# Kernel optimization log

Measured on AMD Instinct MI355X. Metric: run time of the kernel, lower is better.

Reference implementation:

```python
import jax, jax.numpy as jnp
import numpy as np

B, S, D = 2, 2048, 1024
H = 16
HD = D // H  # 64


def setup_inputs() -> dict:
    key = jax.random.key(0)
    k1, k2, k3, k4, k5, k6 = jax.random.split(key, 6)
    hidden_states = jax.random.normal(k1, (B, S, D), dtype=jnp.float32)
    attention_mask = jax.random.randint(k2, (B, S), 0, 2, dtype=jnp.int32)
    scale = 1.0 / np.sqrt(D)
    Wq = jax.random.normal(k3, (D, D), dtype=jnp.float32) * scale
    bq = jax.random.normal(k4, (D,), dtype=jnp.float32) * 0.02
    Wk = jax.random.normal(k5, (D, D), dtype=jnp.float32) * scale
    bk = jax.random.normal(k6, (D,), dtype=jnp.float32) * 0.02
    return {"hidden_states": hidden_states, "attention_mask": attention_mask,
            "Wq": Wq, "bq": bq, "Wk": Wk, "bk": bk}


def _split_heads(x):
    # [B, S, D] -> [B, H, S, HD]
    b, s, _ = x.shape
    return x.reshape(b, s, H, HD).transpose(0, 2, 1, 3)


def reference(hidden_states, attention_mask, Wq, bq, Wk, bk):
    dh = jnp.sqrt(jnp.float32(HD))
    q = _split_heads(hidden_states @ Wq + bq)            # [B,H,S,HD]
    k = _split_heads(hidden_states @ Wk + bk)            # [B,H,S,HD]
    v = q + k                                            # value = Q + K
    k_t = -jax.nn.log_sigmoid(-k)                        # negate the logsigmoid(-K) transform
    scores = jnp.einsum('bhqd,bhkd->bhqk', q, k_t) / dh  # [B,H,S,S]
    # mask applied on the QUERY axis (dim 2), broadcast over key axis (faithful to source)
    mask = (attention_mask[:, None, :, None] == 0)       # [B,1,S,1]
    scores = jnp.where(mask, jnp.float32(-10000.0), scores)
    probs = jax.nn.softmax(scores, axis=-1)              # dropout: eval mode (identity)
    ctx = jnp.einsum('bhqk,bhkd->bhqd', probs, v)        # [B,H,S,HD]
    ctx = ctx.transpose(0, 2, 1, 3).reshape(B, S, D)
    return ctx
```

## Files before the change

kernel.cpp:

```cpp
#include <hip/hip_runtime.h>
#include <hip/hip_bf16.h>

#define B_ 2
#define S_ 2048
#define D_ 1024
#define H_ 16
#define HD_ 64

typedef __attribute__((ext_vector_type(8))) short short8;
typedef __attribute__((ext_vector_type(4))) short short4v;
typedef __attribute__((ext_vector_type(4))) float float4v;

typedef const __attribute__((address_space(1))) void* gas_ptr;
typedef __attribute__((address_space(3))) void* las_ptr;

static __device__ inline void gl_lds16(const void* g, void* l) {
  __builtin_amdgcn_global_load_lds((gas_ptr)g, (las_ptr)l, 16, 0, 0);
}

static __device__ inline short f2bs(float x) {
  __hip_bfloat16 h = __float2bfloat16(x);
  union { __hip_bfloat16 h; short s; } u; u.h = h; return u.s;
}
static __device__ inline float bs2f(short s) {
  union { short s; __hip_bfloat16 h; } u; u.s = s; return __bfloat162float(u.h);
}
static __device__ inline short4v pk4(float a, float b, float c, float d) {
  union { __hip_bfloat162 h[2]; short4v s; } u;
  u.h[0] = __float22bfloat162_rn(float2{a, b});
  u.h[1] = __float22bfloat162_rn(float2{c, d});
  return u.s;
}

static __device__ inline float4v mfma32(short8 a, short8 b, float4v c) {
  return __builtin_amdgcn_mfma_f32_16x16x32_bf16(a, b, c, 0, 0, 0);
}
static __device__ inline float4v mfma16(short4v a, short4v b, float4v c) {
  return __builtin_amdgcn_mfma_f32_16x16x16bf16_1k(a, b, c, 0, 0, 0);
}

__global__ __launch_bounds__(256) void prep(
    const float* __restrict__ hs, __hip_bfloat16* __restrict__ hsb,
    const float* __restrict__ Wq, const float* __restrict__ Wk,
    __hip_bfloat16* __restrict__ Wqt, __hip_bfloat16* __restrict__ Wkt) {
  __shared__ float t[64][65];
  const int id = blockIdx.x;
  if (id < 2048) {
    const size_t i = ((size_t)id * 256 + threadIdx.x) * 8;
    const float4v a0 = ((const float4v*)(hs + i))[0];
    const float4v a1 = ((const float4v*)(hs + i))[1];
    short8 s;
#pragma unroll
    for (int j = 0; j < 4; ++j) { s[j] = f2bs(a0[j]); s[4 + j] = f2bs(a1[j]); }
    *(short8*)(hsb + i) = s;
    return;
  }
  const int bid = id - 2048;
  const float* W = (bid >> 8) ? Wk : Wq;
  __hip_bfloat16* Wt = (bid >> 8) ? Wkt : Wqt;
  const int n0 = (bid & 15) * 64, k0 = ((bid >> 4) & 15) * 64;
  const int c = threadIdx.x & 63, r0 = threadIdx.x >> 6;
  for (int i = 0; i < 16; ++i) {
    const int r = i * 4 + r0;
    t[c][r] = W[(size_t)(k0 + r) * D_ + n0 + c];
  }
  __syncthreads();
  for (int i = 0; i < 16; ++i) {
    const int rr = i * 4 + r0;
    Wt[(size_t)(n0 + rr) * D_ + k0 + c] = __float2bfloat16(t[rr][c]);
  }
}

__global__ __launch_bounds__(256, 2) void gemm_fused(
    const __hip_bfloat16* __restrict__ hsb,
    const __hip_bfloat16* __restrict__ Wqt, const __hip_bfloat16* __restrict__ Wkt,
    const float* __restrict__ bq, const float* __restrict__ bk,
    __hip_bfloat16* __restrict__ q_out, __hip_bfloat16* __restrict__ kt_out,
    __hip_bfloat16* __restrict__ vT) {
  const int id = blockIdx.x;
  const int mt = (id & 7) * 8 + ((id >> 3) & 7);
  const int nt = id >> 6;
  const int n0 = nt * 128, m0 = mt * 64;
  __shared__ __hip_bfloat16 As[2][64 * 32];
  __shared__ __hip_bfloat16 Bq[2][128 * 32];
  __shared__ __hip_bfloat16 Bk[2][128 * 32];
  const int tid = threadIdx.x, wid = tid >> 6, lane = tid & 63;
  const int wm = (wid >> 1) * 32, wn = (wid & 1) * 64;
  const int l15 = lane & 15, l4 = lane >> 4;
  const float4v zz = {0.f, 0.f, 0.f, 0.f};
  float4v accq[2][4], acck[2][4];
  for (int i = 0; i < 2; ++i)
    for (int j = 0; j < 4; ++j) { accq[i][j] = zz; acck[i][j] = zz; }
  const int lrow = wid * 16 + (lane >> 2);
  const int lk8 = (((lane & 3) ^ ((lane >> 3) & 3)) * 8);
  {
    gl_lds16(hsb + (size_t)(m0 + lrow) * D_ + lk8, As[0] + wid * 512);
    gl_lds16(Wqt + (size_t)(n0 + lrow) * D_ + lk8, Bq[0] + wid * 512);
    gl_lds16(Wqt + (size_t)(n0 + 64 + lrow) * D_ + lk8, Bq[0] + 2048 + wid * 512);
    gl_lds16(Wkt + (size_t)(n0 + lrow) * D_ + lk8, Bk[0] + wid * 512);
    gl_lds16(Wkt + (size_t)(n0 + 64 + lrow) * D_ + lk8, Bk[0] + 2048 + wid * 512);
  }
  int p = 0;
  for (int kb = 0; kb < 32; ++kb) {
    __syncthreads();
    if (kb < 31) {
      const int kc = (kb + 1) * 32 + lk8;
      gl_lds16(hsb + (size_t)(m0 + lrow) * D_ + kc, As[p ^ 1] + wid * 512);
      gl_lds16(Wqt + (size_t)(n0 + lrow) * D_ + kc, Bq[p ^ 1] + wid * 512);
      gl_lds16(Wqt + (size_t)(n0 + 64 + lrow) * D_ + kc, Bq[p ^ 1] + 2048 + wid * 512);
      gl_lds16(Wkt + (size_t)(n0 + lrow) * D_ + kc, Bk[p ^ 1] + wid * 512);
      gl_lds16(Wkt + (size_t)(n0 + 64 + lrow) * D_ + kc, Bk[p ^ 1] + 2048 + wid * 512);
    }
    short8 af[2], bfq[4], bfk[4];
    const int fo = ((l4 ^ ((l15 >> 1) & 3)) * 8);
    for (int rt = 0; rt < 2; ++rt)
      af[rt] = *(const short8*)(As[p] + (wm + rt * 16 + l15) * 32 + fo);
    for (int ct = 0; ct < 4; ++ct) {
      bfq[ct] = *(const short8*)(Bq[p] + (wn + ct * 16 + l15) * 32 + fo);
      bfk[ct] = *(const short8*)(Bk[p] + (wn + ct * 16 + l15) * 32 + fo);
    }
    for (int rt = 0; rt < 2; ++rt)
      for (int ct = 0; ct < 4; ++ct) {
        accq[rt][ct] = mfma32(af[rt], bfq[ct], accq[rt][ct]);
        acck[rt][ct] = mfma32(af[rt], bfk[ct], acck[rt][ct]);
      }
    p ^= 1;
  }
  float bvq[4], bvk[4];
  for (int ct = 0; ct < 4; ++ct) {
    bvq[ct] = bq[n0 + wn + ct * 16 + l15];
    bvk[ct] = bk[n0 + wn + ct * 16 + l15];
  }
  for (int rt = 0; rt < 2; ++rt)
    for (int ct = 0; ct < 4; ++ct) {
      const int col = n0 + wn + ct * 16 + l15;
      const int h = col >> 6, d = col & 63;
      const int rowb = m0 + wm + rt * 16 + l4 * 4;
      short4v vv;
      for (int r = 0; r < 4; ++r) {
        const int row = rowb + r;
        const float qv = accq[rt][ct][r] + bvq[ct];
        const float kv = acck[rt][ct][r] + bvk[ct];
        const float sp = fmaxf(kv, 0.f) + __logf(1.f + __expf(-fabsf(kv)));
        q_out[(size_t)row * D_ + col] = __float2bfloat16(qv);
        kt_out[(size_t)row * D_ + col] = __float2bfloat16(sp);
        vv[r] = f2bs(qv + kv);
      }
      const int b = rowb >> 11, s = rowb & 2047;
      const int sw = (s & ~63) | (((s >> 4) & 3) << 2) | (((s >> 2) & 3) << 4);
      *(short4v*)(vT + ((size_t)(b * H_ + h) * HD_ + d) * S_ + sw) = vv;
    }
}

__global__ __launch_bounds__(256, 2) void attn(
    const __hip_bfloat16* __restrict__ qb, const __hip_bfloat16* __restrict__ ktb,
    const __hip_bfloat16* __restrict__ vT, const int* __restrict__ mask,
    float* __restrict__ out) {
  __shared__ short smem[32768];
  const int id = blockIdx.x;
  const int xcd = id & 7;
  const int rest = id >> 3;
  const int q0 = (rest & 15) * 128;
  const int hb = (rest >> 4) * 8 + xcd;
  const int h = hb >> 1, b = hb & 1;
  const int tid = threadIdx.x, wid = tid >> 6, lane = tid & 63;
  const int l15 = lane & 15, l4 = lane >> 4;
  const int qs = (wid & 1) * 64;
  const int kh = wid >> 1;
  const __hip_bfloat16* qh = qb + (size_t)b * S_ * D_ + h * HD_;
  const __hip_bfloat16* kh_ = ktb + (size_t)b * S_ * D_ + h * HD_;
  const __hip_bfloat16* vh = vT + (size_t)(b * H_ + h) * HD_ * S_;
  const int srow = tid >> 2;
  const int b0 = tid & 3;
  const int ssw = ((srow & 1) << 2) | ((srow >> 1) & 3);
  const int w0 = srow * 64 + ((b0 ^ ssw) * 8);
  const int w1 = srow * 64 + (((b0 + 4) ^ ssw) * 8);

  const float SC = 0.125f * 1.44269504f;
  short8 bq0[4], bq1[4];
#pragma unroll
  for (int T = 0; T < 4; ++T) {
    const int qr = q0 + qs + T * 16 + l15;
    const float mq = (mask[b * S_ + qr] != 0) ? SC : 0.f;
    const short8 r0 = *(const short8*)(qh + (size_t)qr * D_ + l4 * 8);
    const short8 r1 = *(const short8*)(qh + (size_t)qr * D_ + 32 + l4 * 8);
#pragma unroll
    for (int j = 0; j < 8; ++j) {
      bq0[T][j] = f2bs(bs2f(r0[j]) * mq);
      bq1[T][j] = f2bs(bs2f(r1[j]) * mq);
    }
  }

  const int lsw = ((l15 & 1) << 2) | ((l15 >> 1) & 3);
  const int ak0off = l15 * 64 + ((l4 ^ lsw) * 8);
  const int ak1off = l15 * 64 + (((l4 + 4) ^ lsw) * 8);
  const int vb0off = ((2 * l4) ^ lsw) * 8;
  const int vb1off = ((2 * l4 + 1) ^ lsw) * 8;

  const float4v zz = {0.f, 0.f, 0.f, 0.f};
  float4v oacc[4][4];
#pragma unroll
  for (int T = 0; T < 4; ++T)
#pragma unroll
    for (int dt = 0; dt < 4; ++dt) oacc[T][dt] = zz;
  float4v ls[4] = {zz, zz, zz, zz};

  short8 gk0[2], gk1[2], gv0[2], gv1[2];
#pragma unroll
  for (int u = 0; u < 2; ++u) {
    gk0[u] = *(const short8*)(kh_ + (size_t)(u * 64 + srow) * D_ + b0 * 8);
    gk1[u] = *(const short8*)(kh_ + (size_t)(u * 64 + srow) * D_ + b0 * 8 + 32);
    gv0[u] = *(const short8*)(vh + (size_t)srow * S_ + u * 64 + b0 * 8);
    gv1[u] = *(const short8*)(vh + (size_t)srow * S_ + u * 64 + b0 * 8 + 32);
  }

  int pb = 0;
  for (int c = 0; c < 16; ++c) {
    short* bufp = smem + pb * 16384;
#pragma unroll
    for (int u = 0; u < 2; ++u) {
      *(short8*)(bufp + u * 4096 + w0) = gk0[u];
      *(short8*)(bufp + u * 4096 + w1) = gk1[u];
      *(short8*)(bufp + 8192 + u * 4096 + w0) = gv0[u];
      *(short8*)(bufp + 8192 + u * 4096 + w1) = gv1[u];
    }
    __syncthreads();
    if (c < 15) {
      const int kb = (c + 1) * 128;
#pragma unroll
      for (int u = 0; u < 2; ++u) {
        gk0[u] = *(const short8*)(kh_ + (size_t)(kb + u * 64 + srow) * D_ + b0 * 8);
        gk1[u] = *(const short8*)(kh_ + (size_t)(kb + u * 64 + srow) * D_ + b0 * 8 + 32);
        gv0[u] = *(const short8*)(vh + (size_t)srow * S_ + kb + u * 64 + b0 * 8);
        gv1[u] = *(const short8*)(vh + (size_t)srow * S_ + kb + u * 64 + b0 * 8 + 32);
      }
    }
    const short* kbase = bufp + kh * 4096;
    const short* vbase = bufp + 8192 + kh * 4096;
    short4v pf[4][4];
#pragma unroll
    for (int t = 0; t < 4; ++t) {
      const short8 ak0 = *(const short8*)(kbase + t * 1024 + ak0off);
      const short8 ak1 = *(const short8*)(kbase + t * 1024 + ak1off);
#pragma unroll
      for (int T = 0; T < 4; ++T) {
        float4v cc = zz;
        cc = mfma32(ak0, bq0[T], cc);
        cc = mfma32(ak1, bq1[T], cc);
        float e[4];
#pragma unroll
        for (int r = 0; r < 4; ++r) {
          e[r] = __builtin_amdgcn_exp2f(cc[r]); ls[T][r] += e[r];
        }
        pf[T][t] = pk4(e[0], e[1], e[2], e[3]);
      }
    }
#pragma unroll
    for (int dt = 0; dt < 4; ++dt) {
      const int rb = (dt * 16 + l15) * 64;
      const short8 av0 = *(const short8*)(vbase + rb + vb0off);
      const short8 av1 = *(const short8*)(vbase + rb + vb1off);
      const short4v a0 = {av0[0], av0[1], av0[2], av0[3]};
      const short4v a1 = {av0[4], av0[5], av0[6], av0[7]};
      const short4v a2 = {av1[0], av1[1], av1[2], av1[3]};
      const short4v a3 = {av1[4], av1[5], av1[6], av1[7]};
#pragma unroll
      for (int T = 0; T < 4; ++T) {
        oacc[T][dt] = mfma16(a0, pf[T][0], oacc[T][dt]);
        oacc[T][dt] = mfma16(a1, pf[T][1], oacc[T][dt]);
        oacc[T][dt] = mfma16(a2, pf[T][2], oacc[T][dt]);
        oacc[T][dt] = mfma16(a3, pf[T][3], oacc[T][dt]);
      }
    }
    pb ^= 1;
  }
  float lT[4];
#pragma unroll
  for (int T = 0; T < 4; ++T) {
    lT[T] = (ls[T][0] + ls[T][1]) + (ls[T][2] + ls[T][3]);
    lT[T] += __shfl_xor(lT[T], 16);
    lT[T] += __shfl_xor(lT[T], 32);
  }
  __syncthreads();
  float* mbuf = (float*)smem;
  float* mlb = (float*)smem + 128 * 68;
  if (kh == 0) {
#pragma unroll
    for (int T = 0; T < 4; ++T) {
      const int row = qs + T * 16 + l15;
#pragma unroll
      for (int dt = 0; dt < 4; ++dt)
        *(float4v*)&mbuf[row * 68 + dt * 16 + l4 * 4] = oacc[T][dt];
      if (l4 == 0) mlb[row] = lT[T];
    }
  }
  __syncthreads();
  if (kh == 1) {
#pragma unroll
    for (int T = 0; T < 4; ++T) {
      const int row = qs + T * 16 + l15;
#pragma unroll
      for (int dt = 0; dt < 4; ++dt) {
        float4v v = *(const float4v*)&mbuf[row * 68 + dt * 16 + l4 * 4];
        v += oacc[T][dt];
        *(float4v*)&mbuf[row * 68 + dt * 16 + l4 * 4] = v;
      }
      if (l4 == 0) mlb[row] += lT[T];
    }
  }
  __syncthreads();
  const int qq = tid & 127;
  const int dg = (tid >> 7) * 32;
  const float li = 1.f / mlb[qq];
  float* orow = out + (size_t)(b * S_ + q0 + qq) * D_ + h * HD_ + dg;
#pragma unroll
  for (int i = 0; i < 8; ++i) {
    float4v v = *(const float4v*)&mbuf[qq * 68 + dg + i * 4];
#pragma unroll
    for (int r = 0; r < 4; ++r) v[r] *= li;
    *(float4v*)(orow + i * 4) = v;
  }
}

extern "C" void kernel_launch(void* const* d_in, const int* in_sizes, int n_in,
                              void* d_out, int out_size, void* d_ws, size_t ws_size,
                              hipStream_t stream) {
  const float* hs = (const float*)d_in[0];
  const int* mask = (const int*)d_in[1];
  const float* Wq = (const float*)d_in[2];
  const float* bq = (const float*)d_in[3];
  const float* Wk = (const float*)d_in[4];
  const float* bk = (const float*)d_in[5];
  float* out = (float*)d_out;
  char* ws = (char*)d_ws;
  const size_t MB = 1u << 20;
  __hip_bfloat16* q_b = (__hip_bfloat16*)(ws + 0 * MB);
  __hip_bfloat16* k_b = (__hip_bfloat16*)(ws + 8 * MB);
  __hip_bfloat16* vT  = (__hip_bfloat16*)(ws + 16 * MB);
  __hip_bfloat16* Wqt = (__hip_bfloat16*)(ws + 24 * MB);
  __hip_bfloat16* Wkt = (__hip_bfloat16*)(ws + 26 * MB);
  __hip_bfloat16* hsb = (__hip_bfloat16*)(ws + 28 * MB);

  prep<<<dim3(2560), 256, 0, stream>>>(hs, hsb, Wq, Wk, Wqt, Wkt);
  gemm_fused<<<dim3(512), 256, 0, stream>>>(hsb, Wqt, Wkt, bq, bk, q_b, k_b, vT);
  attn<<<dim3(512), 256, 0, stream>>>(q_b, k_b, vT, mask, out);
}
```

Measured before the change: 158.1 us.

## Split attention key range across blocks and add a combine kernel

The attention kernel now splits the key sequence into two halves handled by separate blocks, each with 4 waves over 32 query rows, giving 1024 blocks and a smaller shared-memory footprint. Partial unnormalized outputs and row sums go to workspace, and a new combine kernel adds the halves and normalizes. This raises occupancy and parallelism, and removes the intra-block cross-wave reduction. In exchange it adds an extra kernel launch and a round-trip of fp32 partials through global memory. The partial buffer reuses workspace regions that earlier kernels used for weights.

New measurement: 166.9 us. 5.6% more time.

```diff
diff --git a/kernel.cpp b/kernel.cpp
--- a/kernel.cpp
+++ b/kernel.cpp
@@ -152,21 +152,24 @@
     }
 }
 
-__global__ __launch_bounds__(256, 2) void attn(
+__global__ __launch_bounds__(256, 4) void attn(
     const __hip_bfloat16* __restrict__ qb, const __hip_bfloat16* __restrict__ ktb,
     const __hip_bfloat16* __restrict__ vT, const int* __restrict__ mask,
-    float* __restrict__ out) {
-  __shared__ short smem[32768];
+    float* __restrict__ po, float* __restrict__ pl) {
+  __shared__ short smem[17408];
   const int id = blockIdx.x;
   const int xcd = id & 7;
   const int rest = id >> 3;
-  const int q0 = (rest & 15) * 128;
-  const int hb = (rest >> 4) * 8 + xcd;
+  const int qt = rest & 15;
+  const int kr = (rest >> 4) & 1;
+  const int hb = (rest >> 5) * 8 + xcd;
   const int h = hb >> 1, b = hb & 1;
+  const int q0 = qt * 128;
+  const int k0 = kr * 1024;
+  const int pid = hb * 16 + qt;
   const int tid = threadIdx.x, wid = tid >> 6, lane = tid & 63;
   const int l15 = lane & 15, l4 = lane >> 4;
-  const int qs = (wid & 1) * 64;
-  const int kh = wid >> 1;
+  const int qs = wid * 32;
   const __hip_bfloat16* qh = qb + (size_t)b * S_ * D_ + h * HD_;
   const __hip_bfloat16* kh_ = ktb + (size_t)b * S_ * D_ + h * HD_;
   const __hip_bfloat16* vh = vT + (size_t)(b * H_ + h) * HD_ * S_;
@@ -177,9 +180,9 @@
   const int w1 = srow * 64 + (((b0 + 4) ^ ssw) * 8);
 
   const float SC = 0.125f * 1.44269504f;
-  short8 bq0[4], bq1[4];
-#pragma unroll
-  for (int T = 0; T < 4; ++T) {
+  short8 bq0[2], bq1[2];
+#pragma unroll
+  for (int T = 0; T < 2; ++T) {
     const int qr = q0 + qs + T * 16 + l15;
     const float mq = (mask[b * S_ + qr] != 0) ? SC : 0.f;
     const short8 r0 = *(const short8*)(qh + (size_t)qr * D_ + l4 * 8);
@@ -198,52 +201,43 @@
   const int vb1off = ((2 * l4 + 1) ^ lsw) * 8;
 
   const float4v zz = {0.f, 0.f, 0.f, 0.f};
-  float4v oacc[4][4];
-#pragma unroll
-  for (int T = 0; T < 4; ++T)
+  float4v oacc[2][4];
+#pragma unroll
+  for (int T = 0; T < 2; ++T)
 #pragma unroll
     for (int dt = 0; dt < 4; ++dt) oacc[T][dt] = zz;
-  float4v ls[4] = {zz, zz, zz, zz};
-
-  short8 gk0[2], gk1[2], gv0[2], gv1[2];
-#pragma unroll
-  for (int u = 0; u < 2; ++u) {
-    gk0[u] = *(const short8*)(kh_ + (size_t)(u * 64 + srow) * D_ + b0 * 8);
-    gk1[u] = *(const short8*)(kh_ + (size_t)(u * 64 + srow) * D_ + b0 * 8 + 32);
-    gv0[u] = *(const short8*)(vh + (size_t)srow * S_ + u * 64 + b0 * 8);
-    gv1[u] = *(const short8*)(vh + (size_t)srow * S_ + u * 64 + b0 * 8 + 32);
-  }
+  float4v ls[2] = {zz, zz};
+
+  short8 gk0, gk1, gv0, gv1;
+  gk0 = *(const short8*)(kh_ + (size_t)(k0 + srow) * D_ + b0 * 8);
+  gk1 = *(const short8*)(kh_ + (size_t)(k0 + srow) * D_ + b0 * 8 + 32);
+  gv0 = *(const short8*)(vh + (size_t)srow * S_ + k0 + b0 * 8);
+  gv1 = *(const short8*)(vh + (size_t)srow * S_ + k0 + b0 * 8 + 32);
 
   int pb = 0;
   for (int c = 0; c < 16; ++c) {
-    short* bufp = smem + pb * 16384;
-#pragma unroll
-    for (int u = 0; u < 2; ++u) {
-      *(short8*)(bufp + u * 4096 + w0) = gk0[u];
-      *(short8*)(bufp + u * 4096 + w1) = gk1[u];
-      *(short8*)(bufp + 8192 + u * 4096 + w0) = gv0[u];
-      *(short8*)(bufp + 8192 + u * 4096 + w1) = gv1[u];
-    }
+    short* bufp = smem + pb * 8192;
+    *(short8*)(bufp + w0) = gk0;
+    *(short8*)(bufp + w1) = gk1;
+    *(short8*)(bufp + 4096 + w0) = gv0;
+    *(short8*)(bufp + 4096 + w1) = gv1;
     __syncthreads();
     if (c < 15) {
-      const int kb = (c + 1) * 128;
-#pragma unroll
-      for (int u = 0; u < 2; ++u) {
-        gk0[u] = *(const short8*)(kh_ + (size_t)(kb + u * 64 + srow) * D_ + b0 * 8);
-        gk1[u] = *(const short8*)(kh_ + (size_t)(kb + u * 64 + srow) * D_ + b0 * 8 + 32);
-        gv0[u] = *(const short8*)(vh + (size_t)srow * S_ + kb + u * 64 + b0 * 8);
-        gv1[u] = *(const short8*)(vh + (size_t)srow * S_ + kb + u * 64 + b0 * 8 + 32);
-      }
-    }
-    const short* kbase = bufp + kh * 4096;
-    const short* vbase = bufp + 8192 + kh * 4096;
-    short4v pf[4][4];
+      const int kb = k0 + (c + 1) * 64;
+      gk0 = *(const short8*)(kh_ + (size_t)(kb + srow) * D_ + b0 * 8);
+      gk1 = *(const short8*)(kh_ + (size_t)(kb + srow) * D_ + b0 * 8 + 32);
+      gv0 = *(const short8*)(vh + (size_t)srow * S_ + kb + b0 * 8);
+      gv1 = *(const short8*)(vh + (size_t)srow * S_ + kb + b0 * 8 + 32);
+    }
+    const short* kbase = bufp;
+    const short* vbase = bufp + 4096;
+    short4v pf[2][4];
 #pragma unroll
     for (int t = 0; t < 4; ++t) {
       const short8 ak0 = *(const short8*)(kbase + t * 1024 + ak0off);
       const short8 ak1 = *(const short8*)(kbase + t * 1024 + ak1off);
 #pragma unroll
-      for (int T = 0; T < 4; ++T) {
+      for (int T = 0; T < 2; ++T) {
         float4v cc = zz;
         cc = mfma32(ak0, bq0[T], cc);
         cc = mfma32(ak1, bq1[T], cc);
@@ -265,7 +259,7 @@
       const short4v a2 = {av1[0], av1[1], av1[2], av1[3]};
       const short4v a3 = {av1[4], av1[5], av1[6], av1[7]};
 #pragma unroll
-      for (int T = 0; T < 4; ++T) {
+      for (int T = 0; T < 2; ++T) {
         oacc[T][dt] = mfma16(a0, pf[T][0], oacc[T][dt]);
         oacc[T][dt] = mfma16(a1, pf[T][1], oacc[T][dt]);
         oacc[T][dt] = mfma16(a2, pf[T][2], oacc[T][dt]);
@@ -274,51 +268,54 @@
     }
     pb ^= 1;
   }
-  float lT[4];
-#pragma unroll
-  for (int T = 0; T < 4; ++T) {
+  float lT[2];
+#pragma unroll
+  for (int T = 0; T < 2; ++T) {
     lT[T] = (ls[T][0] + ls[T][1]) + (ls[T][2] + ls[T][3]);
     lT[T] += __shfl_xor(lT[T], 16);
     lT[T] += __shfl_xor(lT[T], 32);
   }
   __syncthreads();
   float* mbuf = (float*)smem;
-  float* mlb = (float*)smem + 128 * 68;
-  if (kh == 0) {
-#pragma unroll
-    for (int T = 0; T < 4; ++T) {
-      const int row = qs + T * 16 + l15;
-#pragma unroll
-      for (int dt = 0; dt < 4; ++dt)
-        *(float4v*)&mbuf[row * 68 + dt * 16 + l4 * 4] = oacc[T][dt];
-      if (l4 == 0) mlb[row] = lT[T];
-    }
+#pragma unroll
+  for (int T = 0; T < 2; ++T) {
+    const int row = qs + T * 16 + l15;
+#pragma unroll
+    for (int dt = 0; dt < 4; ++dt)
+      *(float4v*)&mbuf[row * 68 + dt * 16 + l4 * 4] = oacc[T][dt];
+    if (l4 == 0) pl[(size_t)(kr * 512 + pid) * 128 + row] = lT[T];
   }
   __syncthreads();
-  if (kh == 1) {
-#pragma unroll
-    for (int T = 0; T < 4; ++T) {
-      const int row = qs + T * 16 + l15;
-#pragma unroll
-      for (int dt = 0; dt < 4; ++dt) {
-        float4v v = *(const float4v*)&mbuf[row * 68 + dt * 16 + l4 * 4];
-        v += oacc[T][dt];
-        *(float4v*)&mbuf[row * 68 + dt * 16 + l4 * 4] = v;
-      }
-      if (l4 == 0) mlb[row] += lT[T];
-    }
-  }
-  __syncthreads();
-  const int qq = tid & 127;
-  const int dg = (tid >> 7) * 32;
-  const float li = 1.f / mlb[qq];
-  float* orow = out + (size_t)(b * S_ + q0 + qq) * D_ + h * HD_ + dg;
+  float* pbase = po + (size_t)(kr * 512 + pid) * 8192 + qs * 64;
 #pragma unroll
   for (int i = 0; i < 8; ++i) {
-    float4v v = *(const float4v*)&mbuf[qq * 68 + dg + i * 4];
-#pragma unroll
-    for (int r = 0; r < 4; ++r) v[r] *= li;
-    *(float4v*)(orow + i * 4) = v;
+    const int e = i * 256 + lane * 4;
+    const int row = qs + (e >> 6), col = e & 63;
+    *(float4v*)(pbase + e) = *(const float4v*)&mbuf[row * 68 + col];
+  }
+}
+
+__global__ __launch_bounds__(256) void comb(
+    const float* __restrict__ po, const float* __restrict__ pl,
+    float* __restrict__ out) {
+  const int pid = blockIdx.x;
+  const int t = threadIdx.x;
+  const int qt = pid & 15, hb = pid >> 4;
+  const int h = hb >> 1, bb = hb & 1;
+  const float* p0 = po + (size_t)pid * 8192;
+  const float* p1 = po + (size_t)(512 + pid) * 8192;
+  const float* l0 = pl + (size_t)pid * 128;
+  const float* l1 = pl + (size_t)(512 + pid) * 128;
+#pragma unroll
+  for (int i = 0; i < 8; ++i) {
+    const int e = i * 1024 + t * 4;
+    const int row = e >> 6, col = e & 63;
+    float4v a = *(const float4v*)(p0 + e);
+    const float4v bv = *(const float4v*)(p1 + e);
+    const float li = 1.f / (l0[row] + l1[row]);
+#pragma unroll
+    for (int r = 0; r < 4; ++r) a[r] = (a[r] + bv[r]) * li;
+    *(float4v*)(out + (size_t)(bb * S_ + qt * 128 + row) * D_ + h * HD_ + col) = a;
   }
 }
 
@@ -340,8 +337,11 @@
   __hip_bfloat16* Wqt = (__hip_bfloat16*)(ws + 24 * MB);
   __hip_bfloat16* Wkt = (__hip_bfloat16*)(ws + 26 * MB);
   __hip_bfloat16* hsb = (__hip_bfloat16*)(ws + 28 * MB);
+  float* po = (float*)(ws + 24 * MB);
+  float* pl = (float*)(ws + 56 * MB);
 
   prep<<<dim3(2560), 256, 0, stream>>>(hs, hsb, Wq, Wk, Wqt, Wkt);
   gemm_fused<<<dim3(512), 256, 0, stream>>>(hsb, Wqt, Wkt, bq, bk, q_b, k_b, vT);
-  attn<<<dim3(512), 256, 0, stream>>>(q_b, k_b, vT, mask, out);
-}
+  attn<<<dim3(1024), 256, 0, stream>>>(q_b, k_b, vT, mask, po, pl);
+  comb<<<dim3(512), 256, 0, stream>>>(po, pl, out);
+}
```
